# Performance work log

Hardware: AMD Instinct MI355X
Metric: run time of the kernel (lower is better)

The kernel has to match this reference:

```python
import jax, jax.numpy as jnp
import numpy as np

N = 4096        # nodes
E = 131072      # edges (avg degree 32)
IN = 512        # in_channels
HID = 512       # hidden_channels
HEADS = 4       # GAT heads
LAYERS = 3      # residual GCN layers
G = 16          # graphs in batch
OUT = 1         # out_channels
NEG_SLOPE = 0.2 # GAT LeakyReLU slope


def setup_inputs() -> dict:
    key = jax.random.key(0)
    ks = jax.random.split(key, 9)
    s = 0.02
    x = jax.random.normal(ks[0], (N, IN), dtype=jnp.float32)
    edge_index = jax.random.randint(ks[1], (2, E), 0, N)
    batch = jnp.sort(jax.random.randint(ks[2], (N,), 0, G))
    W_gat = jax.random.normal(ks[3], (HEADS, IN, HID), dtype=jnp.float32) * s
    a_src = jax.random.normal(ks[4], (HEADS, HID), dtype=jnp.float32) * s
    a_dst = jax.random.normal(ks[5], (HEADS, HID), dtype=jnp.float32) * s
    W_gcn = jax.random.normal(ks[6], (LAYERS, HID, HID), dtype=jnp.float32) * s
    fc_w = jax.random.normal(ks[7], (HID, OUT), dtype=jnp.float32) * s
    fc_b = jnp.zeros((OUT,), dtype=jnp.float32)
    return {"x": x, "edge_index": edge_index, "batch": batch,
            "W_gat": W_gat, "a_src": a_src, "a_dst": a_dst,
            "W_gcn": W_gcn, "fc_w": fc_w, "fc_b": fc_b}


def reference(x, edge_index, batch, W_gat, a_src, a_dst, W_gcn, fc_w, fc_b):
    src, dst = edge_index[0], edge_index[1]

    # ---- LatentRelationCapturerGAT: multi-head GAT, one output per head ----
    h = jnp.einsum('nc,hcd->nhd', x, W_gat)                    # [N,H,D]
    lg_src = jnp.einsum('nhd,hd->nh', h, a_src)                # [N,H]
    lg_dst = jnp.einsum('nhd,hd->nh', h, a_dst)                # [N,H]
    e = jax.nn.leaky_relu(lg_src[src] + lg_dst[dst], NEG_SLOPE)  # [E,H]
    # segment softmax over incoming edges of each destination node
    m = jax.ops.segment_max(e, dst, num_segments=N)            # [N,H]
    w = jnp.exp(e - m[dst])                                    # [E,H]
    z = jax.ops.segment_sum(w, dst, num_segments=N)            # [N,H]
    alpha = w / (z[dst] + 1e-16)                               # [E,H]
    H0 = jax.ops.segment_sum(alpha[:, :, None] * h[src], dst, num_segments=N)  # [N,H,D]

    # ---- dense adjacency build + GCN normalization (shared across heads) ----
    A = jnp.zeros((N, N), dtype=x.dtype).at[src, dst].set(1.0)
    A = A + jnp.eye(N, dtype=x.dtype)                          # self-loops
    dinv = jax.lax.rsqrt(jnp.sum(A, axis=1))                   # deg >= 1
    A_hat = dinv[:, None] * A * dinv[None, :]                  # D^-1/2 (A+I) D^-1/2

    # ---- DeepResidualGCN: H <- relu(A_hat @ H @ W_l) + H (heads batched) ----
    H = H0
    for l in range(W_gcn.shape[0]):
        P = jnp.einsum('nm,mhd->nhd', A_hat, H)                # propagate
        H = jax.nn.relu(jnp.einsum('nhd,de->nhe', P, W_gcn[l])) + H

    # ---- per-head global mean pool, then mean over heads ----
    ones = jnp.ones((N,), dtype=x.dtype)
    cnt = jnp.maximum(jax.ops.segment_sum(ones, batch, num_segments=G), 1.0)  # [G]
    pooled = jax.ops.segment_sum(H, batch, num_segments=G) / cnt[:, None, None]  # [G,H,D]
    feats = pooled.mean(axis=1)                                # [G,D]

    return feats @ fc_w + fc_b                                 # [G,OUT]
```

## Files before the change

### kernel.cpp

```cpp
#include <hip/hip_runtime.h>
#include <cstdint>
#include <cstddef>

#define Nn    4096
#define Ee    131072
#define INC   512
#define HIDC  512
#define HEADS 4
#define NLAY  3
#define GG    16
#define FW    2048

typedef __attribute__((ext_vector_type(8))) short bfrag;
typedef __attribute__((ext_vector_type(4))) float ffrag;

__device__ __forceinline__ ushort f2bf(float v){
  uint u = __builtin_bit_cast(uint, v);
  u += 0x7fffu + ((u>>16)&1u);
  return (ushort)(u>>16);
}
__device__ __forceinline__ float bf2f(ushort s){
  uint u = ((uint)s)<<16; return __builtin_bit_cast(float, u);
}
__device__ __forceinline__ void fma8(float* acc, uint4 g, float w){
  uint u[4] = {g.x, g.y, g.z, g.w};
  #pragma unroll
  for (int q=0;q<4;q++){
    float lo = __builtin_bit_cast(float, u[q]<<16);
    float hi = __builtin_bit_cast(float, u[q] & 0xffff0000u);
    acc[2*q]   += w*lo;
    acc[2*q+1] += w*hi;
  }
}
__device__ __forceinline__ void pack8(void* p, const float* a){
  uint4 o;
  o.x = (uint)f2bf(a[0]) | ((uint)f2bf(a[1])<<16);
  o.y = (uint)f2bf(a[2]) | ((uint)f2bf(a[3])<<16);
  o.z = (uint)f2bf(a[4]) | ((uint)f2bf(a[5])<<16);
  o.w = (uint)f2bf(a[6]) | ((uint)f2bf(a[7])<<16);
  *(uint4*)p = o;
}

__global__ __launch_bounds__(256) void prep(
    const float* __restrict__ x, ushort* __restrict__ Xb,
    const float* __restrict__ Wgat, ushort* __restrict__ Tgat,
    const float* __restrict__ Wgcn, ushort* __restrict__ Tgcn,
    const int* __restrict__ src, const int* __restrict__ dst,
    int* __restrict__ indeg, unsigned int* __restrict__ bitmap,
    int* __restrict__ cnt_s, int* __restrict__ flag){
  __shared__ float tile[32][33];
  int b = blockIdx.x, t = threadIdx.x;
  if (b < 8192){
    int i = b*256 + t;
    Xb[i] = f2bf(x[i]);
  } else if (b < 9984){
    int idx = b - 8192;
    int z = idx >> 8, xy = idx & 255;
    const float* W; ushort* T; int bb;
    if (z < 4){ W = Wgat; T = Tgat; bb = z; } else { W = Wgcn; T = Tgcn; bb = z-4; }
    int r0 = (xy>>4)*32, c0 = (xy&15)*32;
    int i = t>>3, j0 = (t&7)*4;
    const float* Wb = W + (size_t)bb*512*512;
    float4 v = *(const float4*)(Wb + (size_t)(r0+i)*512 + c0 + j0);
    tile[i][j0]=v.x; tile[i][j0+1]=v.y; tile[i][j0+2]=v.z; tile[i][j0+3]=v.w;
    __syncthreads();
    ushort* o = T + (size_t)bb*512*512 + (size_t)(c0+i)*512 + r0 + j0;
    #pragma unroll
    for (int q=0;q<4;q++) o[q] = f2bf(tile[j0+q][i]);
  } else {
    int e = (b-9984)*256 + t; if (e>=Ee) return;
    int s = src[e], d = dst[e];
    atomicAdd(&indeg[d],1);
    unsigned int key = (unsigned int)s*Nn + (unsigned int)d;
    unsigned int bit = 1u<<(key&31);
    unsigned int old = atomicOr(&bitmap[key>>5], bit);
    int f = (old & bit) ? 0 : 1;
    flag[e] = f;
    if (f) atomicAdd(&cnt_s[s],1);
  }
}

__global__ __launch_bounds__(256) void gemm_bf(
    const ushort* __restrict__ A, const ushort* __restrict__ B,
    const ushort* Res, ushort* Cb,
    int M, int N, int K, int relu_res)
{
  __shared__ __align__(16) ushort Ah[2][2048];
  __shared__ __align__(16) ushort Bh[2][4096];
  int t = threadIdx.x;
  int m0 = blockIdx.y*64, n0 = blockIdx.x*128;
  int srA = t>>2, kqA = t&3;
  const ushort* pA = A + (size_t)(m0+srA)*K + kqA*8;
  int wA = (kqA*64 + srA)*8;
  int srB = t>>1, cB = t&1;
  const ushort* pB = B + (size_t)(n0+srB)*K + cB*16;
  int wB0 = ((2*cB)*128 + srB)*8;
  int wB1 = wB0 + 1024;

  int wave = t>>6, lane = t&63;
  int wm = (wave&1)*32, wn = (wave>>1)*64;
  int lm = lane&15, quad = lane>>4;

  ffrag acc[2][4];
  #pragma unroll
  for (int i=0;i<2;i++){
    #pragma unroll
    for (int j=0;j<4;j++) acc[i][j] = (ffrag){0.f,0.f,0.f,0.f};
  }

  uint4 ra  = *(const uint4*)(pA);
  uint4 rb0 = *(const uint4*)(pB);  uint4 rb1 = *(const uint4*)(pB+8);
  *(uint4*)&Ah[0][wA]  = ra;
  *(uint4*)&Bh[0][wB0] = rb0; *(uint4*)&Bh[0][wB1] = rb1;
  if (K > 32){
    ra  = *(const uint4*)(pA+32);
    rb0 = *(const uint4*)(pB+32); rb1 = *(const uint4*)(pB+40);
  }
  __syncthreads();

  for (int k0 = 0; k0 < K; k0 += 32){
    int cur = (k0>>5)&1, nxt = cur^1;
    bfrag af[2];
    #pragma unroll
    for (int mt=0; mt<2; mt++)
      af[mt] = *(const bfrag*)&Ah[cur][(quad*64 + wm + mt*16 + lm)*8];
    #pragma unroll
    for (int nt=0; nt<4; nt++){
      bfrag bf = *(const bfrag*)&Bh[cur][(quad*128 + wn + nt*16 + lm)*8];
      #pragma unroll
      for (int mt=0; mt<2; mt++)
        acc[mt][nt] = __builtin_amdgcn_mfma_f32_16x16x32_bf16(af[mt], bf, acc[mt][nt], 0,0,0);
    }
    if (k0+32 < K){
      *(uint4*)&Ah[nxt][wA]  = ra;
      *(uint4*)&Bh[nxt][wB0] = rb0; *(uint4*)&Bh[nxt][wB1] = rb1;
      if (k0+64 < K){
        ra  = *(const uint4*)(pA+k0+64);
        rb0 = *(const uint4*)(pB+k0+64); rb1 = *(const uint4*)(pB+k0+72);
      }
    }
    __syncthreads();
  }

  #pragma unroll
  for (int mt=0; mt<2; mt++){
    #pragma unroll
    for (int nt=0; nt<4; nt++){
      #pragma unroll
      for (int r=0;r<4;r++){
        int grow = m0 + wm + mt*16 + quad*4 + r;
        int gcol = n0 + wn + nt*16 + lm;
        size_t off = (size_t)grow*N + gcol;
        float v = acc[mt][nt][r];
        if (relu_res) v = fmaxf(v,0.f) + bf2f(Res[off]);
        Cb[off] = f2bf(v);
      }
    }
  }
}

__global__ __launch_bounds__(256) void compute_lg(const ushort* __restrict__ hbf,
    const float* __restrict__ a_src, const float* __restrict__ a_dst,
    float* __restrict__ lgs, float* __restrict__ lgd){
  int n = blockIdx.x; int t = threadIdx.x;
  int hd = t>>6, lane = t&63;
  uint4 g = *(const uint4*)(hbf + (size_t)n*FW + hd*HIDC + lane*8);
  float h[8] = {0,0,0,0,0,0,0,0};
  fma8(h, g, 1.0f);
  float4 as0 = *(const float4*)(a_src + hd*HIDC + lane*8);
  float4 as1 = *(const float4*)(a_src + hd*HIDC + lane*8 + 4);
  float4 ad0 = *(const float4*)(a_dst + hd*HIDC + lane*8);
  float4 ad1 = *(const float4*)(a_dst + hd*HIDC + lane*8 + 4);
  float s1 = h[0]*as0.x + h[1]*as0.y + h[2]*as0.z + h[3]*as0.w
           + h[4]*as1.x + h[5]*as1.y + h[6]*as1.z + h[7]*as1.w;
  float s2 = h[0]*ad0.x + h[1]*ad0.y + h[2]*ad0.z + h[3]*ad0.w
           + h[4]*ad1.x + h[5]*ad1.y + h[6]*ad1.z + h[7]*ad1.w;
  for (int off=32; off; off>>=1){ s1 += __shfl_down(s1,off); s2 += __shfl_down(s2,off); }
  if (lane==0){ lgs[n*HEADS+hd]=s1; lgd[n*HEADS+hd]=s2; }
}

__global__ __launch_bounds__(1024) void scan3(const int* __restrict__ indeg, int* __restrict__ rp_d,
    const int* __restrict__ cnt_s, int* __restrict__ rp_s, float* __restrict__ dinv,
    const int* __restrict__ batch, int* __restrict__ goff){
  __shared__ int sums[1024];
  __shared__ int cnt2[GG];
  int t = threadIdx.x;
  if (blockIdx.x == 2){
    if (t<GG) cnt2[t]=0;
    __syncthreads();
    for (int i=t;i<Nn;i+=1024) atomicAdd(&cnt2[batch[i]],1);
    __syncthreads();
    if (t==0){ int run=0; for (int g=0; g<GG; g++){ goff[g]=run; run+=cnt2[g]; } goff[GG]=run; }
    return;
  }
  const int* cnt = blockIdx.x ? cnt_s : indeg;
  int* rowptr    = blockIdx.x ? rp_s  : rp_d;
  int v[4]; int s=0;
  #pragma unroll
  for (int i=0;i<4;i++){ int idx=t*4+i; v[i] = cnt[idx]; s+=v[i]; }
  sums[t]=s; __syncthreads();
  for (int off=1; off<1024; off<<=1){
    int other = (t>=off)? sums[t-off] : 0;
    __syncthreads();
    sums[t] += other;
    __syncthreads();
  }
  int run = (t>0)? sums[t-1] : 0;
  #pragma unroll
  for (int i=0;i<4;i++){
    int idx=t*4+i; rowptr[idx]=run; run+=v[i];
    if (blockIdx.x) dinv[idx] = 1.0f/sqrtf((float)(1+v[i]));
  }
  if (t==1023) rowptr[Nn]=sums[1023];
}

__global__ __launch_bounds__(256) void edge_pass2(const int* __restrict__ src, const int* __restrict__ dst,
    const int* __restrict__ flag,
    const int* __restrict__ rp_d, int* __restrict__ fill_d, int* __restrict__ slist,
    const int* __restrict__ rp_s, int* __restrict__ fill_s, int2* __restrict__ cw,
    const float* __restrict__ dinv){
  int e = blockIdx.x*256+threadIdx.x; if (e>=Ee) return;
  int s = src[e], d = dst[e];
  int p = atomicAdd(&fill_d[d],1); slist[rp_d[d]+p] = s;
  if (flag[e]){
    int q = atomicAdd(&fill_s[s],1);
    cw[rp_s[s]+q] = make_int2(d, __float_as_int(dinv[d]));
  }
}

__global__ __launch_bounds__(256) void gat_aggregate(const ushort* __restrict__ hbf,
    const float* __restrict__ lgs, const float* __restrict__ lgd,
    const int* __restrict__ rowptr, const int* __restrict__ slist,
    ushort* __restrict__ Hbf){
  int t = threadIdx.x;
  int wv = __builtin_amdgcn_readfirstlane(t>>6);
  int lane = t&63;
  int b = blockIdx.x;
  int hd = __builtin_amdgcn_readfirstlane(b & 3);
  int n = ((b>>2)<<2) + wv;
  int beg = __builtin_amdgcn_readfirstlane(rowptr[n]);
  int end = __builtin_amdgcn_readfirstlane(rowptr[n+1]);
  int deg = end - beg;
  float ldst = lgd[n*HEADS+hd];
  float m_ = -3.4e38f, z_ = 0.f;
  for (int i=lane; i<deg; i+=64){
    int s = slist[beg+i];
    float v = lgs[s*HEADS+hd] + ldst;
    v = v>0.f ? v : 0.2f*v;
    float mn = fmaxf(m_, v);
    z_ = z_*__expf(m_-mn) + __expf(v-mn);
    m_ = mn;
  }
  for (int o=32;o;o>>=1){
    float mo = __shfl_down(m_,o), zo = __shfl_down(z_,o);
    float mn = fmaxf(m_, mo);
    z_ = z_*__expf(m_-mn) + zo*__expf(mo-mn);
    m_ = mn;
  }
  float mx = __shfl(m_,0);
  float zs = __shfl(z_,0);
  float inv = 1.f/(zs+1e-16f);
  float acc[8] = {0,0,0,0,0,0,0,0};
  const ushort* hb = hbf + hd*HIDC + lane*8;
  int i = beg;
  if (i+4 <= end){
    uint4 g0[4]; float lv0[4];
    #pragma unroll
    for (int q=0;q<4;q++){
      int s = slist[i+q];
      g0[q] = *(const uint4*)(hb + (size_t)s*FW);
      lv0[q] = lgs[s*HEADS+hd];
    }
    i += 4;
    for (; i+4<=end; i+=4){
      uint4 g1[4]; float lv1[4];
      #pragma unroll
      for (int q=0;q<4;q++){
        int s = slist[i+q];
        g1[q] = *(const uint4*)(hb + (size_t)s*FW);
        lv1[q] = lgs[s*HEADS+hd];
      }
      #pragma unroll
      for (int q=0;q<4;q++){
        float v = lv0[q] + ldst; v = v>0.f ? v : 0.2f*v;
        fma8(acc, g0[q], __expf(v-mx)*inv);
      }
      #pragma unroll
      for (int q=0;q<4;q++){ g0[q]=g1[q]; lv0[q]=lv1[q]; }
    }
    #pragma unroll
    for (int q=0;q<4;q++){
      float v = lv0[q] + ldst; v = v>0.f ? v : 0.2f*v;
      fma8(acc, g0[q], __expf(v-mx)*inv);
    }
  }
  for (; i<end; i++){
    int s = slist[i];
    uint4 g = *(const uint4*)(hb + (size_t)s*FW);
    float v = lgs[s*HEADS+hd] + ldst; v = v>0.f ? v : 0.2f*v;
    fma8(acc, g, __expf(v-mx)*inv);
  }
  size_t off = (size_t)n*FW + hd*HIDC + lane*8;
  pack8(Hbf + off, acc);
}

__global__ __launch_bounds__(256) void spmm_bf(const ushort* __restrict__ Hbf,
    ushort* __restrict__ Phi,
    const int* __restrict__ rowptr, const int2* __restrict__ cw, const float* __restrict__ dinv){
  int t = threadIdx.x;
  int wv = __builtin_amdgcn_readfirstlane(t>>6);
  int lane = t&63;
  int b = blockIdx.x;
  int ck = __builtin_amdgcn_readfirstlane(b & 3);
  int n = ((b>>2)<<2) + wv;
  int f = (ck<<9) + lane*8;
  float di = dinv[n];
  float acc[8] = {0,0,0,0,0,0,0,0};
  const ushort* hb = Hbf + f;
  uint4 self = *(const uint4*)(hb + (size_t)n*FW);
  fma8(acc, self, di*di);
  int beg = __builtin_amdgcn_readfirstlane(rowptr[n]);
  int end = __builtin_amdgcn_readfirstlane(rowptr[n+1]);
  int i = beg;
  if (i+4 <= end){
    int2 e0[4]; uint4 g0[4];
    #pragma unroll
    for (int q=0;q<4;q++) e0[q] = cw[i+q];
    #pragma unroll
    for (int q=0;q<4;q++) g0[q] = *(const uint4*)(hb + (size_t)e0[q].x*FW);
    i += 4;
    for (; i+4<=end; i+=4){
      int2 e1[4]; uint4 g1[4];
      #pragma unroll
      for (int q=0;q<4;q++) e1[q] = cw[i+q];
      #pragma unroll
      for (int q=0;q<4;q++) g1[q] = *(const uint4*)(hb + (size_t)e1[q].x*FW);
      #pragma unroll
      for (int q=0;q<4;q++) fma8(acc, g0[q], di*__int_as_float(e0[q].y));
      #pragma unroll
      for (int q=0;q<4;q++){ e0[q]=e1[q]; g0[q]=g1[q]; }
    }
    #pragma unroll
    for (int q=0;q<4;q++) fma8(acc, g0[q], di*__int_as_float(e0[q].y));
  }
  for (; i<end; i++){
    int2 e = cw[i];
    uint4 g = *(const uint4*)(hb + (size_t)e.x*FW);
    fma8(acc, g, di*__int_as_float(e.y));
  }
  pack8(Phi + (size_t)n*FW + f, acc);
}

__global__ __launch_bounds__(256) void pool_accum(const ushort* __restrict__ Hb,
    const int* __restrict__ batch, float* __restrict__ psum){
  int d2 = blockIdx.y*256 + threadIdx.x;
  int n0 = blockIdx.x*32;
  int g = batch[n0];
  float s0 = 0.f, s1 = 0.f;
  for (int k=0;k<32;k++){
    int n = n0+k;
    int gn = batch[n];
    if (gn != g){
      atomicAdd(&psum[(size_t)g*FW + d2*2],   s0);
      atomicAdd(&psum[(size_t)g*FW + d2*2+1], s1);
      s0=0.f; s1=0.f; g=gn;
    }
    uint v = *(const uint*)(Hb + (size_t)n*FW + d2*2);
    s0 += bf2f((ushort)(v&0xffff));
    s1 += bf2f((ushort)(v>>16));
  }
  atomicAdd(&psum[(size_t)g*FW + d2*2],   s0);
  atomicAdd(&psum[(size_t)g*FW + d2*2+1], s1);
}
__global__ __launch_bounds__(256) void final_out(const float* __restrict__ psum,
    const int* __restrict__ goff,
    const float* __restrict__ fc_w, const float* __restrict__ fc_b, float* __restrict__ out){
  int g = blockIdx.x; int t = threadIdx.x;
  float cinv = 0.25f / fmaxf((float)(goff[g+1]-goff[g]), 1.f);
  float p = 0.f;
  for (int d=t; d<HIDC; d+=256){
    float f = cinv*(psum[(size_t)g*FW+d] + psum[(size_t)g*FW+HIDC+d]
                  + psum[(size_t)g*FW+2*HIDC+d] + psum[(size_t)g*FW+3*HIDC+d]);
    p += f*fc_w[d];
  }
  __shared__ float red[4];
  for (int off=32; off; off>>=1) p += __shfl_down(p,off);
  if ((t&63)==0) red[t>>6]=p;
  __syncthreads();
  if (t==0) out[g] = red[0]+red[1]+red[2]+red[3] + fc_b[0];
}

extern "C" void kernel_launch(void* const* d_in, const int* in_sizes, int n_in,
                              void* d_out, int out_size, void* d_ws, size_t ws_size,
                              hipStream_t stream){
  const float* x      = (const float*)d_in[0];
  const int*   ei     = (const int*)d_in[1];
  const int*   batch  = (const int*)d_in[2];
  const float* W_gat  = (const float*)d_in[3];
  const float* a_src  = (const float*)d_in[4];
  const float* a_dst  = (const float*)d_in[5];
  const float* W_gcn  = (const float*)d_in[6];
  const float* fc_w   = (const float*)d_in[7];
  const float* fc_b   = (const float*)d_in[8];
  float* out = (float*)d_out;
  const int* src = ei;
  const int* dst = ei + Ee;

  char* w = (char*)d_ws;
  size_t off = 0;
  auto alloc = [&](size_t bytes)->char*{ char* p = w + off; off = (off + bytes + 255) & ~(size_t)255; return p; };
  ushort* hbf    = (ushort*)alloc((size_t)Nn*FW*2);
  ushort* Hbf    = (ushort*)alloc((size_t)Nn*FW*2);
  ushort* Xbf    = (ushort*)alloc((size_t)Nn*INC*2);
  ushort* WgatT  = (ushort*)alloc((size_t)HEADS*INC*HIDC*2);
  ushort* WgcnT  = (ushort*)alloc((size_t)NLAY*HIDC*HIDC*2);
  float* lgs    = (float*)alloc((size_t)Nn*HEADS*4);
  float* lgd    = (float*)alloc((size_t)Nn*HEADS*4);
  int* indeg    = (int*)alloc(Nn*4);
  int* fill_d   = (int*)alloc(Nn*4);
  int* cnt_s    = (int*)alloc(Nn*4);
  int* fill_s   = (int*)alloc(Nn*4);
  float* psum   = (float*)alloc((size_t)GG*FW*4);
  unsigned int* bitmap = (unsigned int*)alloc((size_t)Nn*Nn/8);
  size_t zero_bytes = (size_t)Nn*4*4 + (size_t)GG*FW*4 + (size_t)Nn*Nn/8;
  int* rowptr_d = (int*)alloc((Nn+1)*4);
  int* slist    = (int*)alloc(Ee*4);
  int* rowptr_s = (int*)alloc((Nn+1)*4);
  int2* cwlist  = (int2*)alloc((size_t)Ee*8);
  int* flag     = (int*)alloc(Ee*4);
  float* dinv   = (float*)alloc(Nn*4);
  int* goff     = (int*)alloc((GG+1)*4);
  ushort* Phi   = hbf;

  hipMemsetAsync(indeg, 0, zero_bytes, stream);

  prep<<<10496,256,0,stream>>>(x, Xbf, W_gat, WgatT, W_gcn, WgcnT,
                               src, dst, indeg, bitmap, cnt_s, flag);

  gemm_bf<<<dim3(FW/128, Nn/64),256,0,stream>>>(Xbf, WgatT,
      nullptr, hbf, Nn, FW, INC, 0);
  compute_lg<<<Nn,256,0,stream>>>(hbf, a_src, a_dst, lgs, lgd);

  scan3<<<3,1024,0,stream>>>(indeg, rowptr_d, cnt_s, rowptr_s, dinv, batch, goff);
  edge_pass2<<<Ee/256,256,0,stream>>>(src, dst, flag, rowptr_d, fill_d, slist,
                                      rowptr_s, fill_s, cwlist, dinv);
  gat_aggregate<<<Nn,256,0,stream>>>(hbf, lgs, lgd, rowptr_d, slist, Hbf);

  for (int l=0;l<NLAY;l++){
    spmm_bf<<<Nn,256,0,stream>>>(Hbf, Phi, rowptr_s, cwlist, dinv);
    gemm_bf<<<dim3(HIDC/128, (Nn*HEADS)/64),256,0,stream>>>(Phi,
        WgcnT + (size_t)l*HIDC*HIDC,
        Hbf, Hbf, Nn*HEADS, HIDC, HIDC, 1);
  }

  pool_accum<<<dim3(Nn/32, FW/512),256,0,stream>>>(Hbf, batch, psum);
  final_out<<<GG,256,0,stream>>>(psum, goff, fc_w, fc_b, out);
}
```

Baseline: 369.6 us.

## Pad GEMM LDS tiles and fuse GAT GEMM with CSR edge fill

Pads the shared-memory row strides of the GEMM A and B tiles (66 and 130 instead of 64 and 128 groups) so fragment reads spread across LDS banks and hit fewer bank conflicts. It also merges the GAT projection GEMM and the edge CSR-fill pass into one launch: scan3 now runs first, and the edge blocks run alongside the GEMM blocks. This removes one kernel launch and lets the latency-bound atomic scatter overlap with MFMA work. The cost is a heterogeneous grid whose edge blocks still reserve the GEMM's shared memory, and a small amount of extra LDS for the padding.

```diff
diff --git a/kernel.cpp b/kernel.cpp
--- a/kernel.cpp
+++ b/kernel.cpp
@@ -10,6 +10,8 @@
 #define NLAY  3
 #define GG    16
 #define FW    2048
+#define ALDS  2112
+#define BLDS  4160
 
 typedef __attribute__((ext_vector_type(8))) short bfrag;
 typedef __attribute__((ext_vector_type(4))) float ffrag;
@@ -80,22 +82,20 @@
   }
 }
 
-__global__ __launch_bounds__(256) void gemm_bf(
+__device__ __forceinline__ void gemm_core(
     const ushort* __restrict__ A, const ushort* __restrict__ B,
     const ushort* Res, ushort* Cb,
-    int M, int N, int K, int relu_res)
+    int M, int N, int K, int relu_res, int m0, int n0,
+    ushort* Ah, ushort* Bh)
 {
-  __shared__ __align__(16) ushort Ah[2][2048];
-  __shared__ __align__(16) ushort Bh[2][4096];
   int t = threadIdx.x;
-  int m0 = blockIdx.y*64, n0 = blockIdx.x*128;
   int srA = t>>2, kqA = t&3;
   const ushort* pA = A + (size_t)(m0+srA)*K + kqA*8;
-  int wA = (kqA*64 + srA)*8;
+  int wA = (kqA*66 + srA)*8;
   int srB = t>>1, cB = t&1;
   const ushort* pB = B + (size_t)(n0+srB)*K + cB*16;
-  int wB0 = ((2*cB)*128 + srB)*8;
-  int wB1 = wB0 + 1024;
+  int wB0 = ((2*cB)*130 + srB)*8;
+  int wB1 = wB0 + 130*8;
 
   int wave = t>>6, lane = t&63;
   int wm = (wave&1)*32, wn = (wave>>1)*64;
@@ -110,8 +110,8 @@
 
   uint4 ra  = *(const uint4*)(pA);
   uint4 rb0 = *(const uint4*)(pB);  uint4 rb1 = *(const uint4*)(pB+8);
-  *(uint4*)&Ah[0][wA]  = ra;
-  *(uint4*)&Bh[0][wB0] = rb0; *(uint4*)&Bh[0][wB1] = rb1;
+  *(uint4*)&Ah[wA]  = ra;
+  *(uint4*)&Bh[wB0] = rb0; *(uint4*)&Bh[wB1] = rb1;
   if (K > 32){
     ra  = *(const uint4*)(pA+32);
     rb0 = *(const uint4*)(pB+32); rb1 = *(const uint4*)(pB+40);
@@ -120,20 +120,22 @@
 
   for (int k0 = 0; k0 < K; k0 += 32){
     int cur = (k0>>5)&1, nxt = cur^1;
+    const ushort* Ac = Ah + cur*ALDS;
+    const ushort* Bc = Bh + cur*BLDS;
     bfrag af[2];
     #pragma unroll
     for (int mt=0; mt<2; mt++)
-      af[mt] = *(const bfrag*)&Ah[cur][(quad*64 + wm + mt*16 + lm)*8];
+      af[mt] = *(const bfrag*)&Ac[(quad*66 + wm + mt*16 + lm)*8];
     #pragma unroll
     for (int nt=0; nt<4; nt++){
-      bfrag bf = *(const bfrag*)&Bh[cur][(quad*128 + wn + nt*16 + lm)*8];
+      bfrag bf = *(const bfrag*)&Bc[(quad*130 + wn + nt*16 + lm)*8];
       #pragma unroll
       for (int mt=0; mt<2; mt++)
         acc[mt][nt] = __builtin_amdgcn_mfma_f32_16x16x32_bf16(af[mt], bf, acc[mt][nt], 0,0,0);
     }
     if (k0+32 < K){
-      *(uint4*)&Ah[nxt][wA]  = ra;
-      *(uint4*)&Bh[nxt][wB0] = rb0; *(uint4*)&Bh[nxt][wB1] = rb1;
+      *(uint4*)&Ah[nxt*ALDS + wA]  = ra;
+      *(uint4*)&Bh[nxt*BLDS + wB0] = rb0; *(uint4*)&Bh[nxt*BLDS + wB1] = rb1;
       if (k0+64 < K){
         ra  = *(const uint4*)(pA+k0+64);
         rb0 = *(const uint4*)(pB+k0+64); rb1 = *(const uint4*)(pB+k0+72);
@@ -155,6 +157,40 @@
         if (relu_res) v = fmaxf(v,0.f) + bf2f(Res[off]);
         Cb[off] = f2bf(v);
       }
+    }
+  }
+}
+
+__global__ __launch_bounds__(256) void gemm_bf(
+    const ushort* __restrict__ A, const ushort* __restrict__ B,
+    const ushort* Res, ushort* Cb,
+    int M, int N, int K, int relu_res)
+{
+  __shared__ __align__(16) ushort Ah[2*ALDS];
+  __shared__ __align__(16) ushort Bh[2*BLDS];
+  gemm_core(A, B, Res, Cb, M, N, K, relu_res, blockIdx.y*64, blockIdx.x*128, Ah, Bh);
+}
+
+__global__ __launch_bounds__(256) void gat_gemm_ep2(
+    const ushort* __restrict__ Xbf, const ushort* __restrict__ WgatT, ushort* __restrict__ hbf,
+    const int* __restrict__ src, const int* __restrict__ dst, const int* __restrict__ flag,
+    const int* __restrict__ rp_d, int* __restrict__ fill_d, int* __restrict__ slist,
+    const int* __restrict__ rp_s, int* __restrict__ fill_s, int2* __restrict__ cw,
+    const float* __restrict__ dinv)
+{
+  __shared__ __align__(16) ushort Ah[2*ALDS];
+  __shared__ __align__(16) ushort Bh[2*BLDS];
+  int b = blockIdx.x;
+  if (b < 1024){
+    int m0 = (b>>4)*64, n0 = (b&15)*128;
+    gemm_core(Xbf, WgatT, nullptr, hbf, Nn, FW, INC, 0, m0, n0, Ah, Bh);
+  } else {
+    int e = (b-1024)*256 + threadIdx.x; if (e>=Ee) return;
+    int s = src[e], d = dst[e];
+    int p = atomicAdd(&fill_d[d],1); slist[rp_d[d]+p] = s;
+    if (flag[e]){
+      int q = atomicAdd(&fill_s[s],1);
+      cw[rp_s[s]+q] = make_int2(d, __float_as_int(dinv[d]));
     }
   }
 }
@@ -212,20 +248,6 @@
     if (blockIdx.x) dinv[idx] = 1.0f/sqrtf((float)(1+v[i]));
   }
   if (t==1023) rowptr[Nn]=sums[1023];
-}
-
-__global__ __launch_bounds__(256) void edge_pass2(const int* __restrict__ src, const int* __restrict__ dst,
-    const int* __restrict__ flag,
-    const int* __restrict__ rp_d, int* __restrict__ fill_d, int* __restrict__ slist,
-    const int* __restrict__ rp_s, int* __restrict__ fill_s, int2* __restrict__ cw,
-    const float* __restrict__ dinv){
-  int e = blockIdx.x*256+threadIdx.x; if (e>=Ee) return;
-  int s = src[e], d = dst[e];
-  int p = atomicAdd(&fill_d[d],1); slist[rp_d[d]+p] = s;
-  if (flag[e]){
-    int q = atomicAdd(&fill_s[s],1);
-    cw[rp_s[s]+q] = make_int2(d, __float_as_int(dinv[d]));
-  }
 }
 
 __global__ __launch_bounds__(256) void gat_aggregate(const ushort* __restrict__ hbf,
@@ -437,13 +459,12 @@
   prep<<<10496,256,0,stream>>>(x, Xbf, W_gat, WgatT, W_gcn, WgcnT,
                                src, dst, indeg, bitmap, cnt_s, flag);
 
-  gemm_bf<<<dim3(FW/128, Nn/64),256,0,stream>>>(Xbf, WgatT,
-      nullptr, hbf, Nn, FW, INC, 0);
+  scan3<<<3,1024,0,stream>>>(indeg, rowptr_d, cnt_s, rowptr_s, dinv, batch, goff);
+
+  gat_gemm_ep2<<<1536,256,0,stream>>>(Xbf, WgatT, hbf,
+      src, dst, flag, rowptr_d, fill_d, slist, rowptr_s, fill_s, cwlist, dinv);
+
   compute_lg<<<Nn,256,0,stream>>>(hbf, a_src, a_dst, lgs, lgd);
-
-  scan3<<<3,1024,0,stream>>>(indeg, rowptr_d, cnt_s, rowptr_s, dinv, batch, goff);
-  edge_pass2<<<Ee/256,256,0,stream>>>(src, dst, flag, rowptr_d, fill_d, slist,
-                                      rowptr_s, fill_s, cwlist, dinv);
   gat_aggregate<<<Nn,256,0,stream>>>(hbf, lgs, lgd, rowptr_d, slist, Hbf);
 
   for (int l=0;l<NLAY;l++){
```

Measured after the change: 361.5 us. -2.2%, faster.
